# Performance work log

Hardware: AMD Instinct MI355X
Metric: run time of the kernel (lower is better)

Reference implementation:

```python
import jax, jax.numpy as jnp
import numpy as np

N = 30000
E = 480000
F_IN = 16
HID = 64
HEADS = 2
D = HID // HEADS
L = 2
NEG_SLOPE = 0.2


def _edge_softmax(alpha, dst, num_nodes):
    # alpha: [E, HEADS]; softmax over edges sharing the same destination node
    amax = jax.ops.segment_max(alpha, dst, num_segments=num_nodes)
    ex = jnp.exp(alpha - amax[dst])
    den = jax.ops.segment_sum(ex, dst, num_segments=num_nodes)
    return ex / (den[dst] + 1e-16)


def _han_edge(x_src, x_dst, ei, a_src, a_dst, n_dst):
    # x_src: [N_src, HEADS, D], x_dst: [N_dst, HEADS, D], ei: [2, E]
    src, dst = ei[0], ei[1]
    a_s = jnp.einsum('nhd,hd->nh', x_src, a_src)
    a_d = jnp.einsum('nhd,hd->nh', x_dst, a_dst)
    alpha = jax.nn.leaky_relu(a_s[src] + a_d[dst], NEG_SLOPE)  # [E, HEADS]
    alpha = _edge_softmax(alpha, dst, n_dst)
    msg = x_src[src] * alpha[..., None]                        # [E, HEADS, D]
    out = jax.ops.segment_sum(msg, dst, num_segments=n_dst)
    return jax.nn.relu(out.reshape(n_dst, HID))


def _group(xs, q, kw, kb):
    # semantic (cross-relation) attention; xs: list of [N, HID]
    out = jnp.stack(xs)                           # [T, N, HID]
    k = jnp.tanh(out @ kw + kb).mean(axis=1)      # [T, HID]
    attn = jax.nn.softmax(jnp.einsum('f,tf->t', q, k))
    return jnp.einsum('t,tnf->nf', attn, out)


def setup_inputs() -> dict:
    key = jax.random.key(0)
    ks = jax.random.split(key, 24)
    s = 0.1
    f32 = jnp.float32
    return {
        'x_job': jax.random.normal(ks[0], (N, F_IN), f32),
        'x_machine': jax.random.normal(ks[1], (N, F_IN), f32),
        'edge_index_jm': jax.random.randint(ks[2], (2, E), 0, N),
        'edge_index_mj': jax.random.randint(ks[3], (2, E), 0, N),
        'edge_index_jj': jax.random.randint(ks[4], (2, E), 0, N),
        'enc_w_job': jax.random.normal(ks[5], (F_IN, HID), f32) * s,
        'enc_b_job': jax.random.normal(ks[6], (HID,), f32) * s,
        'enc_w_machine': jax.random.normal(ks[7], (F_IN, HID), f32) * s,
        'enc_b_machine': jax.random.normal(ks[8], (HID,), f32) * s,
        'proj_w': jax.random.normal(ks[9], (L, 2, HID, HID), f32) * s,
        'proj_b': jax.random.normal(ks[10], (L, 2, HID), f32) * s,
        'att_src': jax.random.normal(ks[11], (L, 3, HEADS, D), f32) * s,
        'att_dst': jax.random.normal(ks[12], (L, 3, HEADS, D), f32) * s,
        'klin_w': jax.random.normal(ks[13], (L, HID, HID), f32) * s,
        'klin_b': jax.random.normal(ks[14], (L, HID), f32) * s,
        'q_sem': jax.random.normal(ks[15], (L, HID), f32) * s,
        'lin0_w': jax.random.normal(ks[16], (HID, HID), f32) * s,
        'lin0_b': jax.random.normal(ks[17], (HID,), f32) * s,
        'linout_w': jax.random.normal(ks[18], (HID, 16), f32) * s,
        'linout_b': jax.random.normal(ks[19], (16,), f32) * s,
        'linv_w': jax.random.normal(ks[20], (HID, 1), f32) * s,
        'linv_b': jax.random.normal(ks[21], (1,), f32) * s,
    }


def reference(x_job, x_machine, edge_index_jm, edge_index_mj, edge_index_jj,
              enc_w_job, enc_b_job, enc_w_machine, enc_b_machine,
              proj_w, proj_b, att_src, att_dst, klin_w, klin_b, q_sem,
              lin0_w, lin0_b, linout_w, linout_b, linv_w, linv_b):
    # per-node-type encoder: Linear + relu_
    xj = jax.nn.relu(x_job @ enc_w_job + enc_b_job)          # [N, HID]
    xm = jax.nn.relu(x_machine @ enc_w_machine + enc_b_machine)
    for l in range(L):
        pj = (xj @ proj_w[l, 0] + proj_b[l, 0]).reshape(N, HEADS, D)
        pm = (xm @ proj_w[l, 1] + proj_b[l, 1]).reshape(N, HEADS, D)
        # edge-type order follows edge_index_dict iteration: jm, mj, jj
        out_jm = _han_edge(pj, pm, edge_index_jm, att_src[l, 0], att_dst[l, 0], N)
        out_mj = _han_edge(pm, pj, edge_index_mj, att_src[l, 1], att_dst[l, 1], N)
        out_jj = _han_edge(pj, pj, edge_index_jj, att_src[l, 2], att_dst[l, 2], N)
        xj = _group([out_mj, out_jj], q_sem[l], klin_w[l], klin_b[l])
        xm = _group([out_jm], q_sem[l], klin_w[l], klin_b[l])
    full_x = jnp.concatenate([xj, xm], axis=0)               # [2N, HID]
    value = (full_x @ linv_w + linv_b).mean()
    h = full_x @ lin0_w + lin0_b
    action = jnp.tanh(h @ linout_w + linout_b)               # [2N, 16]
    return action, value
```

## Files before the change

### kernel.cpp

```cpp
#include <hip/hip_runtime.h>
#include <math.h>


#define GEMM_GRID 256
#define KRED_GRID 128
#define BUCKET_SHIFT 6
#define BUCKET_NODES 64
#define BUCKET_CAP 1536
#define BIN_CHUNK 2048

__device__ __forceinline__ float4 ld4(const float* __restrict__ p, int idx4)
{
    return ((const float4*)p)[idx4];
}

__device__ __forceinline__ float halfred(float v)
{
#pragma unroll
    for (int off = 16; off; off >>= 1) v += __shfl_xor(v, off);
    return v;
}

struct ProjSide {
    const float* x0; const float* x1; const float* attn;
    const float* W; const float* b; float* p;
    const float* a0v; float* o0; const float* a1v; float* o1;
    const float* a2v; float* o2; const float* a3v; float* o3;
};

__global__ __launch_bounds__(256, 4) void proj2_kernel(ProjSide sa, ProjSide sb, int n)
{
    const ProjSide S = blockIdx.y ? sb : sa;
    __shared__ __align__(16) float xs[16][64];
    int tid = threadIdx.x, lane = tid & 63, wid = tid >> 6;
    float Wreg[64];
#pragma unroll
    for (int k = 0; k < 64; k++) Wreg[k] = S.W[k * 64 + lane];
    float bc = S.b[lane];
    float a0c = S.o0 ? S.a0v[lane] : 0.f;
    float a1c = S.o1 ? S.a1v[lane] : 0.f;
    float a2c = S.o2 ? S.a2v[lane] : 0.f;
    float a3c = S.o3 ? S.a3v[lane] : 0.f;
    float ca0 = 0.f, ca1 = 0.f;
    if (S.x1) { ca0 = S.attn[0]; ca1 = S.attn[1]; }
    int qn = tid >> 4, qq = tid & 15;
    for (int base = blockIdx.x * 16; base < n; base += gridDim.x * 16) {
        __syncthreads();
        int node = base + qn;
        if (node < n) {
            float4 xq;
            if (S.x1) {
                float4 u = ld4(S.x0, node * 16 + qq), v = ld4(S.x1, node * 16 + qq);
                xq.x = ca0 * u.x + ca1 * v.x; xq.y = ca0 * u.y + ca1 * v.y;
                xq.z = ca0 * u.z + ca1 * v.z; xq.w = ca0 * u.w + ca1 * v.w;
            } else {
                xq = ld4(S.x0, node * 16 + qq);
            }
            *(float4*)&xs[qn][qq * 4] = xq;
        }
        __syncthreads();
#pragma unroll
        for (int nd = 0; nd < 4; nd++) {
            int nc = base + wid * 4 + nd;
            if (nc >= n) break;
            float acc = bc;
#pragma unroll
            for (int k4 = 0; k4 < 16; k4++) {
                float4 xv = *(const float4*)&xs[wid * 4 + nd][k4 * 4];
                acc = fmaf(xv.x, Wreg[4 * k4 + 0], acc);
                acc = fmaf(xv.y, Wreg[4 * k4 + 1], acc);
                acc = fmaf(xv.z, Wreg[4 * k4 + 2], acc);
                acc = fmaf(xv.w, Wreg[4 * k4 + 3], acc);
            }
            S.p[nc * 64 + lane] = acc;
            int h = lane >> 5;
            if (S.o0) { float v = halfred(acc * a0c); if ((lane & 31) == 0) S.o0[nc * 2 + h] = v; }
            if (S.o1) { float v = halfred(acc * a1c); if ((lane & 31) == 0) S.o1[nc * 2 + h] = v; }
            if (S.o2) { float v = halfred(acc * a2c); if ((lane & 31) == 0) S.o2[nc * 2 + h] = v; }
            if (S.o3) { float v = halfred(acc * a3c); if ((lane & 31) == 0) S.o3[nc * 2 + h] = v; }
        }
    }
}

struct EncSide {
    const float* x; const float* We; const float* be;
    const float* W; const float* b; float* p;
    const float* a0v; float* o0; const float* a1v; float* o1;
    const float* a2v; float* o2; const float* a3v; float* o3;
};

__global__ __launch_bounds__(256, 4) void encproj2_kernel(EncSide sa, EncSide sb, int n)
{
    const EncSide S = blockIdx.y ? sb : sa;
    __shared__ __align__(16) float xs[16][16];
    __shared__ __align__(16) float es[16][64];
    int tid = threadIdx.x, lane = tid & 63, wid = tid >> 6;
    float Ereg[16];
#pragma unroll
    for (int k = 0; k < 16; k++) Ereg[k] = S.We[k * 64 + lane];
    float Wreg[64];
#pragma unroll
    for (int k = 0; k < 64; k++) Wreg[k] = S.W[k * 64 + lane];
    float ebc = S.be[lane], bc = S.b[lane];
    float a0c = S.o0 ? S.a0v[lane] : 0.f;
    float a1c = S.o1 ? S.a1v[lane] : 0.f;
    float a2c = S.o2 ? S.a2v[lane] : 0.f;
    float a3c = S.o3 ? S.a3v[lane] : 0.f;
    for (int base = blockIdx.x * 16; base < n; base += gridDim.x * 16) {
        __syncthreads();
        if (tid < 64) {
            int nn = tid >> 2, q = tid & 3;
            int node = base + nn;
            if (node < n) *(float4*)&xs[nn][q * 4] = ld4(S.x, node * 4 + q);
        }
        __syncthreads();
#pragma unroll
        for (int nd = 0; nd < 4; nd++) {
            int nc = base + wid * 4 + nd;
            if (nc >= n) break;
            float a = ebc;
#pragma unroll
            for (int k4 = 0; k4 < 4; k4++) {
                float4 xv = *(const float4*)&xs[wid * 4 + nd][k4 * 4];
                a = fmaf(xv.x, Ereg[4 * k4 + 0], a);
                a = fmaf(xv.y, Ereg[4 * k4 + 1], a);
                a = fmaf(xv.z, Ereg[4 * k4 + 2], a);
                a = fmaf(xv.w, Ereg[4 * k4 + 3], a);
            }
            es[wid * 4 + nd][lane] = fmaxf(a, 0.f);
        }
        __syncthreads();
#pragma unroll
        for (int nd = 0; nd < 4; nd++) {
            int nc = base + wid * 4 + nd;
            if (nc >= n) break;
            float acc = bc;
#pragma unroll
            for (int k4 = 0; k4 < 16; k4++) {
                float4 xv = *(const float4*)&es[wid * 4 + nd][k4 * 4];
                acc = fmaf(xv.x, Wreg[4 * k4 + 0], acc);
                acc = fmaf(xv.y, Wreg[4 * k4 + 1], acc);
                acc = fmaf(xv.z, Wreg[4 * k4 + 2], acc);
                acc = fmaf(xv.w, Wreg[4 * k4 + 3], acc);
            }
            S.p[nc * 64 + lane] = acc;
            int h = lane >> 5;
            if (S.o0) { float v = halfred(acc * a0c); if ((lane & 31) == 0) S.o0[nc * 2 + h] = v; }
            if (S.o1) { float v = halfred(acc * a1c); if ((lane & 31) == 0) S.o1[nc * 2 + h] = v; }
            if (S.o2) { float v = halfred(acc * a2c); if ((lane & 31) == 0) S.o2[nc * 2 + h] = v; }
            if (S.o3) { float v = halfred(acc * a3c); if ((lane & 31) == 0) S.o3[nc * 2 + h] = v; }
        }
    }
}

__global__ __launch_bounds__(256) void bin_kernel(
    const int* __restrict__ s0, const int* __restrict__ s1, const int* __restrict__ s2,
    const int* __restrict__ d0, const int* __restrict__ d1, const int* __restrict__ d2,
    int* __restrict__ cursor,
    int* __restrict__ binned,
    int e, int nb)
{
    int ty = blockIdx.y;
    const int* s = ty == 0 ? s0 : (ty == 1 ? s1 : s2);
    const int* d = ty == 0 ? d0 : (ty == 1 ? d1 : d2);
    __shared__ int cnt[512], rbase[512];
    int tid = threadIdx.x;
    for (int i = tid; i < nb; i += 256) cnt[i] = 0;
    __syncthreads();
    int beg = blockIdx.x * BIN_CHUNK;
    int end = beg + BIN_CHUNK; if (end > e) end = e;
    for (int i = beg + tid; i < end; i += 256)
        atomicAdd(&cnt[d[i] >> BUCKET_SHIFT], 1);
    __syncthreads();
    for (int i = tid; i < nb; i += 256) {
        rbase[i] = atomicAdd(&cursor[ty * nb + i], cnt[i]);
        cnt[i] = 0;
    }
    __syncthreads();
    int* bb = binned + (size_t)ty * nb * BUCKET_CAP;
    for (int i = beg + tid; i < end; i += 256) {
        int dv = d[i], b = dv >> BUCKET_SHIFT;
        int slot = rbase[b] + atomicAdd(&cnt[b], 1);
        if (slot < BUCKET_CAP)
            bb[b * BUCKET_CAP + slot] = (s[i] << BUCKET_SHIFT) | (dv & (BUCKET_NODES - 1));
    }
}

__global__ void bucketscan_kernel(const int* __restrict__ cursor,
                                  int* __restrict__ bbase, int nb)
{
    int ty = blockIdx.x;
    const int* c = cursor + (size_t)ty * nb;
    int* o = bbase + (size_t)ty * nb;
    int lane = threadIdx.x;
    int carry = 0;
    for (int base = 0; base < nb; base += 64) {
        int i = base + lane;
        int v = (i < nb) ? c[i] : 0;
        int incl = v;
#pragma unroll
        for (int off = 1; off < 64; off <<= 1) {
            int u = __shfl_up(incl, off);
            if (lane >= off) incl += u;
        }
        if (i < nb) o[i] = carry + incl - v;
        carry += __shfl(incl, 63);
    }
}

__global__ __launch_bounds__(256) void bucket_kernel(
    const int* __restrict__ cursor, const int* __restrict__ bbase,
    const int* __restrict__ binned,
    int* __restrict__ rowptr,
    int* __restrict__ rowend,
    int* __restrict__ colsrc,
    int n, int nb, int e)
{
    int ty = blockIdx.y, b = blockIdx.x;
    __shared__ int stage[BUCKET_CAP];
    __shared__ int ncnt[64], nexcl[64], ncur[64];
    int tid = threadIdx.x;
    int cnt = cursor[ty * nb + b]; if (cnt > BUCKET_CAP) cnt = BUCKET_CAP;
    int base = bbase[ty * nb + b];
    const int* bb = binned + ((size_t)ty * nb + b) * BUCKET_CAP;
    if (tid < 64) ncnt[tid] = 0;
    __syncthreads();
    for (int i = tid; i < cnt; i += 256) {
        int v = bb[i];
        stage[i] = v;
        atomicAdd(&ncnt[v & (BUCKET_NODES - 1)], 1);
    }
    __syncthreads();
    if (tid < 64) {
        int v = ncnt[tid];
        int incl = v;
#pragma unroll
        for (int off = 1; off < 64; off <<= 1) {
            int u = __shfl_up(incl, off);
            if (tid >= off) incl += u;
        }
        int excl = incl - v;
        nexcl[tid] = excl;
        ncur[tid] = 0;
        int node = (b << BUCKET_SHIFT) + tid;
        if (node < n) {
            rowptr[(size_t)ty * n + node] = base + excl;
            rowend[(size_t)ty * n + node] = base + excl + v;
        }
    }
    __syncthreads();
    int* cs = colsrc + (size_t)ty * e;
    for (int i = tid; i < cnt; i += 256) {
        int v = stage[i];
        int dl = v & (BUCKET_NODES - 1);
        int pos = nexcl[dl] + atomicAdd(&ncur[dl], 1);
        cs[base + pos] = v >> BUCKET_SHIFT;
    }
}

struct AggSide {
    const int* rp; const int* re; const int* cs;
    const float* xsrc; const float* as; const float* ad;
    float* out;
};

__global__ __launch_bounds__(256, 8) void agg3_kernel(AggSide A0, AggSide A1, AggSide A2, int n)
{
    const AggSide A = blockIdx.y == 0 ? A0 : (blockIdx.y == 1 ? A1 : A2);
    __shared__ int ebuf[4][96];
    int tid = threadIdx.x;
    int lane = tid & 63, wid = tid >> 6;
    int node = blockIdx.x * 4 + wid;
    if (node >= n) return;
    int l32 = lane & 31;
    int hh = lane >> 5;
    int g = lane >> 4;
    int q = lane & 15;
    int hq = q >> 3;
    int beg = A.rp[node], end = A.re[node];
    float ad = A.ad[node * 2 + hh];
    float den = 0.f;
    float4 acc = {0.f, 0.f, 0.f, 0.f};
    int* eb = ebuf[wid];
    for (int c = beg; c < end; c += 32) {
        int cnt = end - c; if (cnt > 32) cnt = 32;
        int sl = A.cs[c + (l32 < cnt ? l32 : 0)];
        float w = 0.f;
        if (l32 < cnt) {
            float a = A.as[sl * 2 + hh] + ad;
            a = (a > 0.f) ? a : 0.2f * a;
            w = __expf(a);
        }
        den += w;
        if (lane < 32) eb[l32 * 3] = sl;
        eb[l32 * 3 + 1 + hh] = __float_as_int(w);
        int iters = (cnt + 3) >> 2;
        int it = 0;
        for (; it + 2 <= iters; it += 2) {
            int e0 = it * 4 + g, e1 = e0 + 4;
            int sa = eb[e0 * 3];
            float wa = __int_as_float(eb[e0 * 3 + 1 + hq]);
            int sb = eb[e1 * 3];
            float wb = __int_as_float(eb[e1 * 3 + 1 + hq]);
            float4 xa = ld4(A.xsrc, sa * 16 + q);
            float4 xb = ld4(A.xsrc, sb * 16 + q);
            acc.x = fmaf(wa, xa.x, acc.x);
            acc.y = fmaf(wa, xa.y, acc.y);
            acc.z = fmaf(wa, xa.z, acc.z);
            acc.w = fmaf(wa, xa.w, acc.w);
            acc.x = fmaf(wb, xb.x, acc.x);
            acc.y = fmaf(wb, xb.y, acc.y);
            acc.z = fmaf(wb, xb.z, acc.z);
            acc.w = fmaf(wb, xb.w, acc.w);
        }
        if (it < iters) {
            int e0 = it * 4 + g;
            int sa = eb[e0 * 3];
            float wa = __int_as_float(eb[e0 * 3 + 1 + hq]);
            float4 xa = ld4(A.xsrc, sa * 16 + q);
            acc.x = fmaf(wa, xa.x, acc.x);
            acc.y = fmaf(wa, xa.y, acc.y);
            acc.z = fmaf(wa, xa.z, acc.z);
            acc.w = fmaf(wa, xa.w, acc.w);
        }
    }
    acc.x += __shfl_xor(acc.x, 16);
    acc.y += __shfl_xor(acc.y, 16);
    acc.z += __shfl_xor(acc.z, 16);
    acc.w += __shfl_xor(acc.w, 16);
    acc.x += __shfl_xor(acc.x, 32);
    acc.y += __shfl_xor(acc.y, 32);
    acc.z += __shfl_xor(acc.z, 32);
    acc.w += __shfl_xor(acc.w, 32);
    float dtot = halfred(den);
    float dq = __shfl(dtot, (q >= 8) ? 32 : 0);
    if (g == 0) {
        float r = 1.f / (dq + 1e-16f);
        float4 o;
        o.x = fmaxf(acc.x * r, 0.f);
        o.y = fmaxf(acc.y * r, 0.f);
        o.z = fmaxf(acc.z * r, 0.f);
        o.w = fmaxf(acc.w * r, 0.f);
        *(float4*)&A.out[node * 64 + q * 4] = o;
    }
}

__global__ __launch_bounds__(256, 4) void kred2_kernel(
    const float* __restrict__ xin0, const float* __restrict__ xin1,
    const float* __restrict__ kw, const float* __restrict__ kb,
    float* __restrict__ kacc0, float* __restrict__ kacc1, int n)
{
    const float* xin = blockIdx.y ? xin1 : xin0;
    float* kacc = blockIdx.y ? kacc1 : kacc0;
    __shared__ __align__(16) float xs[16][64];
    __shared__ float red[256];
    int tid = threadIdx.x, lane = tid & 63, wid = tid >> 6;
    float Wreg[64];
#pragma unroll
    for (int k = 0; k < 64; k++) Wreg[k] = kw[k * 64 + lane];
    float bc = kb[lane];
    int qn = tid >> 4, qq = tid & 15;
    float kl = 0.f;
    for (int base = blockIdx.x * 16; base < n; base += gridDim.x * 16) {
        __syncthreads();
        int node = base + qn;
        if (node < n) *(float4*)&xs[qn][qq * 4] = ld4(xin, node * 16 + qq);
        __syncthreads();
#pragma unroll
        for (int nd = 0; nd < 4; nd++) {
            int nc = base + wid * 4 + nd;
            if (nc >= n) break;
            float acc = bc;
#pragma unroll
            for (int k4 = 0; k4 < 16; k4++) {
                float4 xv = *(const float4*)&xs[wid * 4 + nd][k4 * 4];
                acc = fmaf(xv.x, Wreg[4 * k4 + 0], acc);
                acc = fmaf(xv.y, Wreg[4 * k4 + 1], acc);
                acc = fmaf(xv.z, Wreg[4 * k4 + 2], acc);
                acc = fmaf(xv.w, Wreg[4 * k4 + 3], acc);
            }
            kl += tanhf(acc);
        }
    }
    red[tid] = kl;
    __syncthreads();
    if (wid == 0) {
        float s = red[lane] + red[64 + lane] + red[128 + lane] + red[192 + lane];
        atomicAdd(&kacc[lane], s);
    }
}

__global__ void attnfin_kernel(const float* __restrict__ kacc, const float* __restrict__ q,
                               float* __restrict__ attn, float inv_n)
{
    int lane = threadIdx.x;
    float qc = q[lane];
    float v0 = qc * kacc[lane] * inv_n;
    float v1 = qc * kacc[64 + lane] * inv_n;
#pragma unroll
    for (int off = 32; off; off >>= 1) {
        v0 += __shfl_xor(v0, off);
        v1 += __shfl_xor(v1, off);
    }
    if (lane == 0) {
        float m = fmaxf(v0, v1);
        float e0 = expf(v0 - m), e1 = expf(v1 - m);
        float inv = 1.f / (e0 + e1);
        attn[0] = e0 * inv;
        attn[1] = e1 * inv;
    }
}

__global__ __launch_bounds__(256, 4) void final_kernel(
    const float* __restrict__ t0, const float* __restrict__ t1,
    const float* __restrict__ attn, const float* __restrict__ xm,
    const float* __restrict__ w0, const float* __restrict__ b0,
    const float* __restrict__ w1, const float* __restrict__ b1,
    const float* __restrict__ wv,
    float* __restrict__ action, float* __restrict__ vsum, int n)
{
    __shared__ __align__(16) float xs[16][64];
    __shared__ __align__(16) float hs[4][4][68];
    __shared__ float W1s[1024];
    __shared__ float red[256];
    int tid = threadIdx.x, lane = tid & 63, wid = tid >> 6;
    int qn = tid >> 4, qq = tid & 15;
    float W0reg[64];
#pragma unroll
    for (int k = 0; k < 64; k++) W0reg[k] = w0[k * 64 + lane];
    float b0c = b0[lane], b1c = b1[lane & 15];
    float ca0 = attn[0], ca1 = attn[1];
    float4 wvq = ld4(wv, qq);
    for (int i = tid; i < 1024; i += 256) W1s[i] = w1[i];
    float vloc = 0.f;
    int n2 = 2 * n;
    for (int base = blockIdx.x * 16; base < n2; base += gridDim.x * 16) {
        __syncthreads();
        int node = base + qn;
        if (node < n2) {
            float4 xq;
            if (node < n) {
                float4 u = ld4(t0, node * 16 + qq), v = ld4(t1, node * 16 + qq);
                xq.x = ca0 * u.x + ca1 * v.x; xq.y = ca0 * u.y + ca1 * v.y;
                xq.z = ca0 * u.z + ca1 * v.z; xq.w = ca0 * u.w + ca1 * v.w;
            } else {
                xq = ld4(xm, (node - n) * 16 + qq);
            }
            *(float4*)&xs[qn][qq * 4] = xq;
            vloc += xq.x * wvq.x + xq.y * wvq.y + xq.z * wvq.z + xq.w * wvq.w;
        }
        __syncthreads();
#pragma unroll
        for (int nd = 0; nd < 4; nd++) {
            int nc = base + wid * 4 + nd;
            if (nc >= n2) break;
            float acc = b0c;
#pragma unroll
            for (int k4 = 0; k4 < 16; k4++) {
                float4 xv = *(const float4*)&xs[wid * 4 + nd][k4 * 4];
                acc = fmaf(xv.x, W0reg[4 * k4 + 0], acc);
                acc = fmaf(xv.y, W0reg[4 * k4 + 1], acc);
                acc = fmaf(xv.z, W0reg[4 * k4 + 2], acc);
                acc = fmaf(xv.w, W0reg[4 * k4 + 3], acc);
            }
            hs[wid][nd][lane] = acc;
        }
        __syncthreads();
        int nd2 = lane >> 4, c2 = lane & 15;
        int nc2 = base + wid * 4 + nd2;
        if (nc2 < n2) {
            float acc2 = b1c;
#pragma unroll
            for (int k4 = 0; k4 < 16; k4++) {
                float4 hv = *(const float4*)&hs[wid][nd2][k4 * 4];
                acc2 = fmaf(hv.x, W1s[(4 * k4 + 0) * 16 + c2], acc2);
                acc2 = fmaf(hv.y, W1s[(4 * k4 + 1) * 16 + c2], acc2);
                acc2 = fmaf(hv.z, W1s[(4 * k4 + 2) * 16 + c2], acc2);
                acc2 = fmaf(hv.w, W1s[(4 * k4 + 3) * 16 + c2], acc2);
            }
            action[(size_t)nc2 * 16 + c2] = tanhf(acc2);
        }
    }
    red[tid] = vloc;
    __syncthreads();
    for (int s = 128; s; s >>= 1) {
        if (tid < s) red[tid] += red[tid + s];
        __syncthreads();
    }
    if (tid == 0) atomicAdd(vsum, red[0]);
}

__global__ void value_finish_kernel(const float* __restrict__ vsum,
                                    const float* __restrict__ vb,
                                    float* __restrict__ out, int twoN)
{
    if (threadIdx.x == 0 && blockIdx.x == 0)
        out[0] = vsum[0] / (float)twoN + vb[0];
}

extern "C" void kernel_launch(void* const* d_in, const int* in_sizes, int n_in,
                              void* d_out, int out_size, void* d_ws, size_t ws_size,
                              hipStream_t stream)
{
    const int N = in_sizes[0] / 16;
    const int E = in_sizes[2] / 2;
    const int NB = (N + BUCKET_NODES - 1) / BUCKET_NODES;

    auto f = [&](int i) { return (const float*)d_in[i]; };
    const float* x_job = f(0);
    const float* x_mac = f(1);
    const int* ei_jm = (const int*)d_in[2];
    const int* ei_mj = (const int*)d_in[3];
    const int* ei_jj = (const int*)d_in[4];
    const float* enc_wj = f(5);
    const float* enc_bj = f(6);
    const float* enc_wm = f(7);
    const float* enc_bm = f(8);
    const float* proj_w = f(9);
    const float* proj_b = f(10);
    const float* att_src = f(11);
    const float* att_dst = f(12);
    const float* klin_w = f(13);
    const float* klin_b = f(14);
    const float* q_sem = f(15);
    const float* lin0_w = f(16);
    const float* lin0_b = f(17);
    const float* lout_w = f(18);
    const float* lout_b = f(19);
    const float* linv_w = f(20);
    const float* linv_b = f(21);

    float* action = (float*)d_out;
    float* value_out = action + (size_t)2 * N * 16;

    char* base = (char*)d_ws;
    size_t off = 0;
    auto alloc = [&](size_t bytes) -> void* {
        void* p = base + off;
        off += (bytes + 255) & ~(size_t)255;
        return p;
    };
    int* cursor3 = (int*)alloc((size_t)3 * NB * 4);
    float* kacc = (float*)alloc(256 * 4);
    float* vsum = (float*)alloc(4);
    size_t zero_bytes = off;

    int* bbase3 = (int*)alloc((size_t)3 * NB * 4);
    int* rowptr3 = (int*)alloc((size_t)3 * N * 4);
    int* rowend3 = (int*)alloc((size_t)3 * N * 4);
    int* colsrc3 = (int*)alloc((size_t)3 * E * 4);
    float* pj = (float*)alloc((size_t)N * 64 * 4);
    float* pm = (float*)alloc((size_t)N * 64 * 4);
    float* out_jm0 = (float*)alloc((size_t)N * 64 * 4);
    float* out_jm1 = (float*)alloc((size_t)N * 64 * 4);
    float* out_mj = (float*)alloc((size_t)N * 64 * 4);
    float* out_jj = (float*)alloc((size_t)N * 64 * 4);
    float* as_jm = (float*)alloc((size_t)N * 2 * 4);
    float* ad_jm = (float*)alloc((size_t)N * 2 * 4);
    float* as_mj = (float*)alloc((size_t)N * 2 * 4);
    float* ad_mj = (float*)alloc((size_t)N * 2 * 4);
    float* as_jj = (float*)alloc((size_t)N * 2 * 4);
    float* ad_jj = (float*)alloc((size_t)N * 2 * 4);
    float* attn0 = (float*)alloc(2 * 4);
    float* attn1 = (float*)alloc(2 * 4);

    int* binned3 = (int*)pj;

    hipMemsetAsync(d_ws, 0, zero_bytes, stream);

    dim3 blk(256);

    int nchunks = (E + BIN_CHUNK - 1) / BIN_CHUNK;
    bin_kernel<<<dim3(nchunks, 3), blk, 0, stream>>>(
        ei_jm, ei_mj, ei_jj, ei_jm + E, ei_mj + E, ei_jj + E,
        cursor3, binned3, E, NB);
    bucketscan_kernel<<<3, 64, 0, stream>>>(cursor3, bbase3, NB);
    bucket_kernel<<<dim3(NB, 3), blk, 0, stream>>>(
        cursor3, bbase3, binned3, rowptr3, rowend3, colsrc3, N, NB, E);

    const int* rp0 = rowptr3;
    const int* rp1 = rowptr3 + N;
    const int* rp2 = rowptr3 + 2 * N;
    const int* re0 = rowend3;
    const int* re1 = rowend3 + N;
    const int* re2 = rowend3 + 2 * N;
    const int* cs0 = colsrc3;
    const int* cs1 = colsrc3 + E;
    const int* cs2 = colsrc3 + 2 * E;

    int ab = (N + 3) / 4;
    float* out_jm_l[2] = {out_jm0, out_jm1};

    for (int l = 0; l < 2; l++) {
        const float* pwj = proj_w + (size_t)(l * 2 + 0) * 4096;
        const float* pwm = proj_w + (size_t)(l * 2 + 1) * 4096;
        const float* pbj = proj_b + (l * 2 + 0) * 64;
        const float* pbm = proj_b + (l * 2 + 1) * 64;
        const float* as0 = att_src + (l * 3 + 0) * 64;
        const float* as1 = att_src + (l * 3 + 1) * 64;
        const float* as2 = att_src + (l * 3 + 2) * 64;
        const float* ad0 = att_dst + (l * 3 + 0) * 64;
        const float* ad1 = att_dst + (l * 3 + 1) * 64;
        const float* ad2 = att_dst + (l * 3 + 2) * 64;

        if (l == 0) {
            EncSide ja = {x_job, enc_wj, enc_bj, pwj, pbj, pj,
                          as0, as_jm, ad1, ad_mj, as2, as_jj, ad2, ad_jj};
            EncSide ma = {x_mac, enc_wm, enc_bm, pwm, pbm, pm,
                          ad0, ad_jm, as1, as_mj, nullptr, nullptr, nullptr, nullptr};
            encproj2_kernel<<<dim3(GEMM_GRID, 2), blk, 0, stream>>>(ja, ma, N);
        } else {
            ProjSide ja = {out_mj, out_jj, attn0, pwj, pbj, pj,
                           as0, as_jm, ad1, ad_mj, as2, as_jj, ad2, ad_jj};
            ProjSide ma = {out_jm0, nullptr, nullptr, pwm, pbm, pm,
                           ad0, ad_jm, as1, as_mj, nullptr, nullptr, nullptr, nullptr};
            proj2_kernel<<<dim3(GEMM_GRID, 2), blk, 0, stream>>>(ja, ma, N);
        }

        AggSide A0 = {rp0, re0, cs0, pj, as_jm, ad_jm, out_jm_l[l]};
        AggSide A1 = {rp1, re1, cs1, pm, as_mj, ad_mj, out_mj};
        AggSide A2 = {rp2, re2, cs2, pj, as_jj, ad_jj, out_jj};
        agg3_kernel<<<dim3(ab, 3), blk, 0, stream>>>(A0, A1, A2, N);

        const float* kw = klin_w + (size_t)l * 4096;
        const float* kb = klin_b + l * 64;
        float* k0 = kacc + l * 128;
        float* k1 = k0 + 64;
        kred2_kernel<<<dim3(KRED_GRID, 2), blk, 0, stream>>>(out_mj, out_jj, kw, kb, k0, k1, N);
        attnfin_kernel<<<1, 64, 0, stream>>>(k0, q_sem + l * 64, l ? attn1 : attn0,
                                             1.f / (float)N);
    }

    final_kernel<<<GEMM_GRID * 2, blk, 0, stream>>>(out_mj, out_jj, attn1, out_jm1,
                                                    lin0_w, lin0_b, lout_w, lout_b, linv_w,
                                                    action, vsum, N);
    value_finish_kernel<<<1, 64, 0, stream>>>(vsum, linv_b, value_out, 2 * N);
}
```

Before: 406.3 us.

## Replace LDS-staged node GEMMs with per-wave direct loads and split combine step

The dense per-node GEMM kernels (projection, encoder+projection, key reduction, final head) stop staging node rows through shared memory behind block barriers. Instead each wave reads its own node's row directly with uniform (readfirstlane) addresses, which gives broadcast loads. The semantic-attention weighted sum becomes a separate combine kernel that writes a materialised buffer. The encoder writes its hidden activations to global memory and reads them back, and grid sizes are doubled. This removes __syncthreads and LDS traffic, but adds extra global round trips and kernel launches, and it drops the occupancy hints from the launch bounds.

```diff
diff --git a/kernel.cpp b/kernel.cpp
--- a/kernel.cpp
+++ b/kernel.cpp
@@ -2,14 +2,15 @@
 #include <math.h>
 
 
-#define GEMM_GRID 256
-#define KRED_GRID 128
+#define GEMM_GRID 512
+#define KRED_GRID 256
+#define FINAL_GRID 1024
 #define BUCKET_SHIFT 6
 #define BUCKET_NODES 64
 #define BUCKET_CAP 1536
 #define BIN_CHUNK 2048
 
-__device__ __forceinline__ float4 ld4(const float* __restrict__ p, int idx4)
+__device__ __forceinline__ float4 ld4(const float* p, int idx4)
 {
     return ((const float4*)p)[idx4];
 }
@@ -21,18 +22,19 @@
     return v;
 }
 
+__device__ __forceinline__ int ufl(int v) { return __builtin_amdgcn_readfirstlane(v); }
+
 struct ProjSide {
-    const float* x0; const float* x1; const float* attn;
-    const float* W; const float* b; float* p;
+    const float* x; const float* W; const float* b; float* p;
     const float* a0v; float* o0; const float* a1v; float* o1;
     const float* a2v; float* o2; const float* a3v; float* o3;
 };
 
-__global__ __launch_bounds__(256, 4) void proj2_kernel(ProjSide sa, ProjSide sb, int n)
+__global__ __launch_bounds__(256) void proj2_kernel(ProjSide sa, ProjSide sb, int n)
 {
     const ProjSide S = blockIdx.y ? sb : sa;
-    __shared__ __align__(16) float xs[16][64];
-    int tid = threadIdx.x, lane = tid & 63, wid = tid >> 6;
+    int tid = threadIdx.x, lane = tid & 63;
+    int wvid = ufl(tid >> 6);
     float Wreg[64];
 #pragma unroll
     for (int k = 0; k < 64; k++) Wreg[k] = S.W[k * 64 + lane];
@@ -41,60 +43,39 @@
     float a1c = S.o1 ? S.a1v[lane] : 0.f;
     float a2c = S.o2 ? S.a2v[lane] : 0.f;
     float a3c = S.o3 ? S.a3v[lane] : 0.f;
-    float ca0 = 0.f, ca1 = 0.f;
-    if (S.x1) { ca0 = S.attn[0]; ca1 = S.attn[1]; }
-    int qn = tid >> 4, qq = tid & 15;
-    for (int base = blockIdx.x * 16; base < n; base += gridDim.x * 16) {
-        __syncthreads();
-        int node = base + qn;
-        if (node < n) {
-            float4 xq;
-            if (S.x1) {
-                float4 u = ld4(S.x0, node * 16 + qq), v = ld4(S.x1, node * 16 + qq);
-                xq.x = ca0 * u.x + ca1 * v.x; xq.y = ca0 * u.y + ca1 * v.y;
-                xq.z = ca0 * u.z + ca1 * v.z; xq.w = ca0 * u.w + ca1 * v.w;
-            } else {
-                xq = ld4(S.x0, node * 16 + qq);
-            }
-            *(float4*)&xs[qn][qq * 4] = xq;
-        }
-        __syncthreads();
-#pragma unroll
-        for (int nd = 0; nd < 4; nd++) {
-            int nc = base + wid * 4 + nd;
-            if (nc >= n) break;
-            float acc = bc;
-#pragma unroll
-            for (int k4 = 0; k4 < 16; k4++) {
-                float4 xv = *(const float4*)&xs[wid * 4 + nd][k4 * 4];
-                acc = fmaf(xv.x, Wreg[4 * k4 + 0], acc);
-                acc = fmaf(xv.y, Wreg[4 * k4 + 1], acc);
-                acc = fmaf(xv.z, Wreg[4 * k4 + 2], acc);
-                acc = fmaf(xv.w, Wreg[4 * k4 + 3], acc);
-            }
-            S.p[nc * 64 + lane] = acc;
-            int h = lane >> 5;
-            if (S.o0) { float v = halfred(acc * a0c); if ((lane & 31) == 0) S.o0[nc * 2 + h] = v; }
-            if (S.o1) { float v = halfred(acc * a1c); if ((lane & 31) == 0) S.o1[nc * 2 + h] = v; }
-            if (S.o2) { float v = halfred(acc * a2c); if ((lane & 31) == 0) S.o2[nc * 2 + h] = v; }
-            if (S.o3) { float v = halfred(acc * a3c); if ((lane & 31) == 0) S.o3[nc * 2 + h] = v; }
-        }
+    int h = lane >> 5;
+    int stride = gridDim.x * 4;
+    for (int node = blockIdx.x * 4 + wvid; node < n; node += stride) {
+        const float* xp = S.x + (size_t)node * 64;
+        float acc = bc;
+#pragma unroll
+        for (int k4 = 0; k4 < 16; k4++) {
+            float4 xq = ld4(xp, k4);
+            acc = fmaf(xq.x, Wreg[4 * k4 + 0], acc);
+            acc = fmaf(xq.y, Wreg[4 * k4 + 1], acc);
+            acc = fmaf(xq.z, Wreg[4 * k4 + 2], acc);
+            acc = fmaf(xq.w, Wreg[4 * k4 + 3], acc);
+        }
+        S.p[(size_t)node * 64 + lane] = acc;
+        if (S.o0) { float v = halfred(acc * a0c); if ((lane & 31) == 0) S.o0[node * 2 + h] = v; }
+        if (S.o1) { float v = halfred(acc * a1c); if ((lane & 31) == 0) S.o1[node * 2 + h] = v; }
+        if (S.o2) { float v = halfred(acc * a2c); if ((lane & 31) == 0) S.o2[node * 2 + h] = v; }
+        if (S.o3) { float v = halfred(acc * a3c); if ((lane & 31) == 0) S.o3[node * 2 + h] = v; }
     }
 }
 
 struct EncSide {
     const float* x; const float* We; const float* be;
-    const float* W; const float* b; float* p;
+    const float* W; const float* b; float* e; float* p;
     const float* a0v; float* o0; const float* a1v; float* o1;
     const float* a2v; float* o2; const float* a3v; float* o3;
 };
 
-__global__ __launch_bounds__(256, 4) void encproj2_kernel(EncSide sa, EncSide sb, int n)
+__global__ __launch_bounds__(256) void encproj2_kernel(EncSide sa, EncSide sb, int n)
 {
     const EncSide S = blockIdx.y ? sb : sa;
-    __shared__ __align__(16) float xs[16][16];
-    __shared__ __align__(16) float es[16][64];
-    int tid = threadIdx.x, lane = tid & 63, wid = tid >> 6;
+    int tid = threadIdx.x, lane = tid & 63;
+    int wvid = ufl(tid >> 6);
     float Ereg[16];
 #pragma unroll
     for (int k = 0; k < 16; k++) Ereg[k] = S.We[k * 64 + lane];
@@ -106,49 +87,61 @@
     float a1c = S.o1 ? S.a1v[lane] : 0.f;
     float a2c = S.o2 ? S.a2v[lane] : 0.f;
     float a3c = S.o3 ? S.a3v[lane] : 0.f;
-    for (int base = blockIdx.x * 16; base < n; base += gridDim.x * 16) {
-        __syncthreads();
-        if (tid < 64) {
-            int nn = tid >> 2, q = tid & 3;
-            int node = base + nn;
-            if (node < n) *(float4*)&xs[nn][q * 4] = ld4(S.x, node * 4 + q);
-        }
-        __syncthreads();
-#pragma unroll
-        for (int nd = 0; nd < 4; nd++) {
-            int nc = base + wid * 4 + nd;
-            if (nc >= n) break;
-            float a = ebc;
-#pragma unroll
-            for (int k4 = 0; k4 < 4; k4++) {
-                float4 xv = *(const float4*)&xs[wid * 4 + nd][k4 * 4];
-                a = fmaf(xv.x, Ereg[4 * k4 + 0], a);
-                a = fmaf(xv.y, Ereg[4 * k4 + 1], a);
-                a = fmaf(xv.z, Ereg[4 * k4 + 2], a);
-                a = fmaf(xv.w, Ereg[4 * k4 + 3], a);
-            }
-            es[wid * 4 + nd][lane] = fmaxf(a, 0.f);
-        }
-        __syncthreads();
-#pragma unroll
-        for (int nd = 0; nd < 4; nd++) {
-            int nc = base + wid * 4 + nd;
-            if (nc >= n) break;
-            float acc = bc;
-#pragma unroll
-            for (int k4 = 0; k4 < 16; k4++) {
-                float4 xv = *(const float4*)&es[wid * 4 + nd][k4 * 4];
-                acc = fmaf(xv.x, Wreg[4 * k4 + 0], acc);
-                acc = fmaf(xv.y, Wreg[4 * k4 + 1], acc);
-                acc = fmaf(xv.z, Wreg[4 * k4 + 2], acc);
-                acc = fmaf(xv.w, Wreg[4 * k4 + 3], acc);
-            }
-            S.p[nc * 64 + lane] = acc;
-            int h = lane >> 5;
-            if (S.o0) { float v = halfred(acc * a0c); if ((lane & 31) == 0) S.o0[nc * 2 + h] = v; }
-            if (S.o1) { float v = halfred(acc * a1c); if ((lane & 31) == 0) S.o1[nc * 2 + h] = v; }
-            if (S.o2) { float v = halfred(acc * a2c); if ((lane & 31) == 0) S.o2[nc * 2 + h] = v; }
-            if (S.o3) { float v = halfred(acc * a3c); if ((lane & 31) == 0) S.o3[nc * 2 + h] = v; }
+    int h = lane >> 5;
+    int stride = gridDim.x * 8;
+    for (int node = (blockIdx.x * 4 + wvid) * 2; node < n; node += stride) {
+        int node1 = (node + 1 < n) ? node + 1 : node;
+        const float* xa = S.x + (size_t)node * 16;
+        const float* xb = S.x + (size_t)node1 * 16;
+        float ea = ebc, eb = ebc;
+#pragma unroll
+        for (int q = 0; q < 4; q++) {
+            float4 u = ld4(xa, q), v = ld4(xb, q);
+            ea = fmaf(u.x, Ereg[4 * q + 0], ea);
+            ea = fmaf(u.y, Ereg[4 * q + 1], ea);
+            ea = fmaf(u.z, Ereg[4 * q + 2], ea);
+            ea = fmaf(u.w, Ereg[4 * q + 3], ea);
+            eb = fmaf(v.x, Ereg[4 * q + 0], eb);
+            eb = fmaf(v.y, Ereg[4 * q + 1], eb);
+            eb = fmaf(v.z, Ereg[4 * q + 2], eb);
+            eb = fmaf(v.w, Ereg[4 * q + 3], eb);
+        }
+        ea = fmaxf(ea, 0.f);
+        eb = fmaxf(eb, 0.f);
+        S.e[(size_t)node * 64 + lane] = ea;
+        S.e[(size_t)node1 * 64 + lane] = eb;
+        const float* ep0 = S.e + (size_t)node * 64;
+        const float* ep1 = S.e + (size_t)node1 * 64;
+        float pa = bc, pb = bc;
+#pragma unroll
+        for (int k4 = 0; k4 < 16; k4++) {
+            float4 u = ld4(ep0, k4), v = ld4(ep1, k4);
+            pa = fmaf(u.x, Wreg[4 * k4 + 0], pa);
+            pa = fmaf(u.y, Wreg[4 * k4 + 1], pa);
+            pa = fmaf(u.z, Wreg[4 * k4 + 2], pa);
+            pa = fmaf(u.w, Wreg[4 * k4 + 3], pa);
+            pb = fmaf(v.x, Wreg[4 * k4 + 0], pb);
+            pb = fmaf(v.y, Wreg[4 * k4 + 1], pb);
+            pb = fmaf(v.z, Wreg[4 * k4 + 2], pb);
+            pb = fmaf(v.w, Wreg[4 * k4 + 3], pb);
+        }
+        S.p[(size_t)node * 64 + lane] = pa;
+        S.p[(size_t)node1 * 64 + lane] = pb;
+        if (S.o0) {
+            float v0 = halfred(pa * a0c), v1 = halfred(pb * a0c);
+            if ((lane & 31) == 0) { S.o0[node * 2 + h] = v0; S.o0[node1 * 2 + h] = v1; }
+        }
+        if (S.o1) {
+            float v0 = halfred(pa * a1c), v1 = halfred(pb * a1c);
+            if ((lane & 31) == 0) { S.o1[node * 2 + h] = v0; S.o1[node1 * 2 + h] = v1; }
+        }
+        if (S.o2) {
+            float v0 = halfred(pa * a2c), v1 = halfred(pb * a2c);
+            if ((lane & 31) == 0) { S.o2[node * 2 + h] = v0; S.o2[node1 * 2 + h] = v1; }
+        }
+        if (S.o3) {
+            float v0 = halfred(pa * a3c), v1 = halfred(pb * a3c);
+            if ((lane & 31) == 0) { S.o3[node * 2 + h] = v0; S.o3[node1 * 2 + h] = v1; }
         }
     }
 }
@@ -156,9 +149,7 @@
 __global__ __launch_bounds__(256) void bin_kernel(
     const int* __restrict__ s0, const int* __restrict__ s1, const int* __restrict__ s2,
     const int* __restrict__ d0, const int* __restrict__ d1, const int* __restrict__ d2,
-    int* __restrict__ cursor,
-    int* __restrict__ binned,
-    int e, int nb)
+    int* __restrict__ cursor, int* __restrict__ binned, int e, int nb)
 {
     int ty = blockIdx.y;
     const int* s = ty == 0 ? s0 : (ty == 1 ? s1 : s2);
@@ -211,9 +202,7 @@
 __global__ __launch_bounds__(256) void bucket_kernel(
     const int* __restrict__ cursor, const int* __restrict__ bbase,
     const int* __restrict__ binned,
-    int* __restrict__ rowptr,
-    int* __restrict__ rowend,
-    int* __restrict__ colsrc,
+    int* __restrict__ rowptr, int* __restrict__ rowend, int* __restrict__ colsrc,
     int n, int nb, int e)
 {
     int ty = blockIdx.y, b = blockIdx.x;
@@ -345,49 +334,35 @@
     }
 }
 
-__global__ __launch_bounds__(256, 4) void kred2_kernel(
-    const float* __restrict__ xin0, const float* __restrict__ xin1,
-    const float* __restrict__ kw, const float* __restrict__ kb,
-    float* __restrict__ kacc0, float* __restrict__ kacc1, int n)
+__global__ __launch_bounds__(256) void kred2_kernel(
+    const float* xin0, const float* xin1,
+    const float* kw, const float* kb,
+    float* kacc0, float* kacc1, int n)
 {
     const float* xin = blockIdx.y ? xin1 : xin0;
     float* kacc = blockIdx.y ? kacc1 : kacc0;
-    __shared__ __align__(16) float xs[16][64];
-    __shared__ float red[256];
-    int tid = threadIdx.x, lane = tid & 63, wid = tid >> 6;
+    int tid = threadIdx.x, lane = tid & 63;
+    int wvid = ufl(tid >> 6);
     float Wreg[64];
 #pragma unroll
     for (int k = 0; k < 64; k++) Wreg[k] = kw[k * 64 + lane];
     float bc = kb[lane];
-    int qn = tid >> 4, qq = tid & 15;
     float kl = 0.f;
-    for (int base = blockIdx.x * 16; base < n; base += gridDim.x * 16) {
-        __syncthreads();
-        int node = base + qn;
-        if (node < n) *(float4*)&xs[qn][qq * 4] = ld4(xin, node * 16 + qq);
-        __syncthreads();
-#pragma unroll
-        for (int nd = 0; nd < 4; nd++) {
-            int nc = base + wid * 4 + nd;
-            if (nc >= n) break;
-            float acc = bc;
-#pragma unroll
-            for (int k4 = 0; k4 < 16; k4++) {
-                float4 xv = *(const float4*)&xs[wid * 4 + nd][k4 * 4];
-                acc = fmaf(xv.x, Wreg[4 * k4 + 0], acc);
-                acc = fmaf(xv.y, Wreg[4 * k4 + 1], acc);
-                acc = fmaf(xv.z, Wreg[4 * k4 + 2], acc);
-                acc = fmaf(xv.w, Wreg[4 * k4 + 3], acc);
-            }
-            kl += tanhf(acc);
-        }
-    }
-    red[tid] = kl;
-    __syncthreads();
-    if (wid == 0) {
-        float s = red[lane] + red[64 + lane] + red[128 + lane] + red[192 + lane];
-        atomicAdd(&kacc[lane], s);
-    }
+    int stride = gridDim.x * 4;
+    for (int node = blockIdx.x * 4 + wvid; node < n; node += stride) {
+        const float* xp = xin + (size_t)node * 64;
+        float acc = bc;
+#pragma unroll
+        for (int k4 = 0; k4 < 16; k4++) {
+            float4 xq = ld4(xp, k4);
+            acc = fmaf(xq.x, Wreg[4 * k4 + 0], acc);
+            acc = fmaf(xq.y, Wreg[4 * k4 + 1], acc);
+            acc = fmaf(xq.z, Wreg[4 * k4 + 2], acc);
+            acc = fmaf(xq.w, Wreg[4 * k4 + 3], acc);
+        }
+        kl += tanhf(acc);
+    }
+    atomicAdd(&kacc[lane], kl);
 }
 
 __global__ void attnfin_kernel(const float* __restrict__ kacc, const float* __restrict__ q,
@@ -411,83 +386,77 @@
     }
 }
 
-__global__ __launch_bounds__(256, 4) void final_kernel(
-    const float* __restrict__ t0, const float* __restrict__ t1,
-    const float* __restrict__ attn, const float* __restrict__ xm,
-    const float* __restrict__ w0, const float* __restrict__ b0,
-    const float* __restrict__ w1, const float* __restrict__ b1,
-    const float* __restrict__ wv,
-    float* __restrict__ action, float* __restrict__ vsum, int n)
-{
-    __shared__ __align__(16) float xs[16][64];
-    __shared__ __align__(16) float hs[4][4][68];
-    __shared__ float W1s[1024];
-    __shared__ float red[256];
-    int tid = threadIdx.x, lane = tid & 63, wid = tid >> 6;
-    int qn = tid >> 4, qq = tid & 15;
+__global__ void combine_kernel(const float* __restrict__ t0, const float* t1,
+                               const float* __restrict__ attn, float* o, int n4)
+{
+    int i = blockIdx.x * blockDim.x + threadIdx.x;
+    if (i >= n4) return;
+    float a0 = attn[0], a1 = attn[1];
+    float4 u = ((const float4*)t0)[i], v = ((const float4*)t1)[i];
+    float4 w;
+    w.x = fmaf(a0, u.x, a1 * v.x);
+    w.y = fmaf(a0, u.y, a1 * v.y);
+    w.z = fmaf(a0, u.z, a1 * v.z);
+    w.w = fmaf(a0, u.w, a1 * v.w);
+    ((float4*)o)[i] = w;
+}
+
+__global__ __launch_bounds__(256) void final_kernel(
+    const float* xj, const float* xm,
+    const float* w0, const float* b0,
+    const float* w1, const float* b1,
+    const float* wvp,
+    float* action, float* vsum, int n)
+{
+    __shared__ float hs[4][4][68];
+    int tid = threadIdx.x, lane = tid & 63;
+    int wvid = ufl(tid >> 6);
     float W0reg[64];
 #pragma unroll
     for (int k = 0; k < 64; k++) W0reg[k] = w0[k * 64 + lane];
+    float W1reg[64];
+#pragma unroll
+    for (int k = 0; k < 64; k++) W1reg[k] = w1[k * 16 + (lane & 15)];
     float b0c = b0[lane], b1c = b1[lane & 15];
-    float ca0 = attn[0], ca1 = attn[1];
-    float4 wvq = ld4(wv, qq);
-    for (int i = tid; i < 1024; i += 256) W1s[i] = w1[i];
+    int n2 = 2 * n;
     float vloc = 0.f;
-    int n2 = 2 * n;
-    for (int base = blockIdx.x * 16; base < n2; base += gridDim.x * 16) {
-        __syncthreads();
-        int node = base + qn;
-        if (node < n2) {
-            float4 xq;
-            if (node < n) {
-                float4 u = ld4(t0, node * 16 + qq), v = ld4(t1, node * 16 + qq);
-                xq.x = ca0 * u.x + ca1 * v.x; xq.y = ca0 * u.y + ca1 * v.y;
-                xq.z = ca0 * u.z + ca1 * v.z; xq.w = ca0 * u.w + ca1 * v.w;
-            } else {
-                xq = ld4(xm, (node - n) * 16 + qq);
+    int stride = gridDim.x * 16;
+    for (int base = (blockIdx.x * 4 + wvid) * 4; base < n2; base += stride) {
+#pragma unroll
+        for (int nd = 0; nd < 4; nd++) {
+            int node = base + nd;
+            if (node >= n2) break;
+            const float* xp = (node < n) ? (xj + (size_t)node * 64)
+                                         : (xm + (size_t)(node - n) * 64);
+            float acc = b0c;
+#pragma unroll
+            for (int k4 = 0; k4 < 16; k4++) {
+                float4 xq = ld4(xp, k4);
+                float4 wq = ld4(wvp, k4);
+                acc = fmaf(xq.x, W0reg[4 * k4 + 0], acc);
+                acc = fmaf(xq.y, W0reg[4 * k4 + 1], acc);
+                acc = fmaf(xq.z, W0reg[4 * k4 + 2], acc);
+                acc = fmaf(xq.w, W0reg[4 * k4 + 3], acc);
+                vloc += xq.x * wq.x + xq.y * wq.y + xq.z * wq.z + xq.w * wq.w;
             }
-            *(float4*)&xs[qn][qq * 4] = xq;
-            vloc += xq.x * wvq.x + xq.y * wvq.y + xq.z * wvq.z + xq.w * wvq.w;
-        }
-        __syncthreads();
-#pragma unroll
-        for (int nd = 0; nd < 4; nd++) {
-            int nc = base + wid * 4 + nd;
-            if (nc >= n2) break;
-            float acc = b0c;
-#pragma unroll
-            for (int k4 = 0; k4 < 16; k4++) {
-                float4 xv = *(const float4*)&xs[wid * 4 + nd][k4 * 4];
-                acc = fmaf(xv.x, W0reg[4 * k4 + 0], acc);
-                acc = fmaf(xv.y, W0reg[4 * k4 + 1], acc);
-                acc = fmaf(xv.z, W0reg[4 * k4 + 2], acc);
-                acc = fmaf(xv.w, W0reg[4 * k4 + 3], acc);
-            }
-            hs[wid][nd][lane] = acc;
-        }
-        __syncthreads();
+            hs[wvid][nd][lane] = acc;
+        }
         int nd2 = lane >> 4, c2 = lane & 15;
-        int nc2 = base + wid * 4 + nd2;
+        int nc2 = base + nd2;
         if (nc2 < n2) {
             float acc2 = b1c;
 #pragma unroll
             for (int k4 = 0; k4 < 16; k4++) {
-                float4 hv = *(const float4*)&hs[wid][nd2][k4 * 4];
-                acc2 = fmaf(hv.x, W1s[(4 * k4 + 0) * 16 + c2], acc2);
-                acc2 = fmaf(hv.y, W1s[(4 * k4 + 1) * 16 + c2], acc2);
-                acc2 = fmaf(hv.z, W1s[(4 * k4 + 2) * 16 + c2], acc2);
-                acc2 = fmaf(hv.w, W1s[(4 * k4 + 3) * 16 + c2], acc2);
+                float4 hv = *(const float4*)&hs[wvid][nd2][k4 * 4];
+                acc2 = fmaf(hv.x, W1reg[4 * k4 + 0], acc2);
+                acc2 = fmaf(hv.y, W1reg[4 * k4 + 1], acc2);
+                acc2 = fmaf(hv.z, W1reg[4 * k4 + 2], acc2);
+                acc2 = fmaf(hv.w, W1reg[4 * k4 + 3], acc2);
             }
             action[(size_t)nc2 * 16 + c2] = tanhf(acc2);
         }
     }
-    red[tid] = vloc;
-    __syncthreads();
-    for (int s = 128; s; s >>= 1) {
-        if (tid < s) red[tid] += red[tid + s];
-        __syncthreads();
-    }
-    if (tid == 0) atomicAdd(vsum, red[0]);
+    if (lane == 0) atomicAdd(vsum, vloc);
 }
 
 __global__ void value_finish_kernel(const float* __restrict__ vsum,
@@ -565,6 +534,10 @@
     float* attn1 = (float*)alloc(2 * 4);
 
     int* binned3 = (int*)pj;
+    float* e_j = out_jm1;
+    float* e_m = out_mj;
+    float* xj1 = out_jm1;
+    float* xjF = out_jj;
 
     hipMemsetAsync(d_ws, 0, zero_bytes, stream);
 
@@ -589,6 +562,7 @@
     const int* cs2 = colsrc3 + 2 * E;
 
     int ab = (N + 3) / 4;
+    int cb = (N * 16 + 255) / 256;
     float* out_jm_l[2] = {out_jm0, out_jm1};
 
     for (int l = 0; l < 2; l++) {
@@ -604,15 +578,16 @@
         const float* ad2 = att_dst + (l * 3 + 2) * 64;
 
         if (l == 0) {
-            EncSide ja = {x_job, enc_wj, enc_bj, pwj, pbj, pj,
+            EncSide ja = {x_job, enc_wj, enc_bj, pwj, pbj, e_j, pj,
                           as0, as_jm, ad1, ad_mj, as2, as_jj, ad2, ad_jj};
-            EncSide ma = {x_mac, enc_wm, enc_bm, pwm, pbm, pm,
+            EncSide ma = {x_mac, enc_wm, enc_bm, pwm, pbm, e_m, pm,
                           ad0, ad_jm, as1, as_mj, nullptr, nullptr, nullptr, nullptr};
             encproj2_kernel<<<dim3(GEMM_GRID, 2), blk, 0, stream>>>(ja, ma, N);
         } else {
-            ProjSide ja = {out_mj, out_jj, attn0, pwj, pbj, pj,
+            combine_kernel<<<cb, blk, 0, stream>>>(out_mj, out_jj, attn0, xj1, N * 16);
+            ProjSide ja = {xj1, pwj, pbj, pj,
                            as0, as_jm, ad1, ad_mj, as2, as_jj, ad2, ad_jj};
-            ProjSide ma = {out_jm0, nullptr, nullptr, pwm, pbm, pm,
+            ProjSide ma = {out_jm0, pwm, pbm, pm,
                            ad0, ad_jm, as1, as_mj, nullptr, nullptr, nullptr, nullptr};
             proj2_kernel<<<dim3(GEMM_GRID, 2), blk, 0, stream>>>(ja, ma, N);
         }
@@ -631,8 +606,9 @@
                                              1.f / (float)N);
     }
 
-    final_kernel<<<GEMM_GRID * 2, blk, 0, stream>>>(out_mj, out_jj, attn1, out_jm1,
-                                                    lin0_w, lin0_b, lout_w, lout_b, linv_w,
-                                                    action, vsum, N);
+    combine_kernel<<<cb, blk, 0, stream>>>(out_mj, out_jj, attn1, xjF, N * 16);
+    final_kernel<<<FINAL_GRID, blk, 0, stream>>>(xjF, out_jm1,
+                                                 lin0_w, lin0_b, lout_w, lout_b, linv_w,
+                                                 action, vsum, N);
     value_finish_kernel<<<1, 64, 0, stream>>>(vsum, linv_b, value_out, 2 * N);
 }
```

Result: slower. 525.7 us (+29.4%).
